# Performance work log

Measured on AMD Instinct MI355X. Metric: run time of the kernel, lower is better.

The kernel has to match this reference:

```python
import jax, jax.numpy as jnp
import numpy as np
import math

B, T, C, H = 2, 2048, 1024, 16

def setup_inputs() -> dict:
    key = jax.random.key(0)
    ks = jax.random.split(key, 5)
    s = 0.02
    return {
        "x": jax.random.normal(ks[0], (B, T, C), dtype=jnp.float32),
        "W_attn": jax.random.normal(ks[1], (C, 3 * C), dtype=jnp.float32) * s,
        "b_attn": jnp.zeros((3 * C,), dtype=jnp.float32),
        "W_proj": jax.random.normal(ks[2], (C, C), dtype=jnp.float32) * s,
        "b_proj": jnp.zeros((C,), dtype=jnp.float32),
    }

def reference(x, W_attn, b_attn, W_proj, b_proj):
    Bx, Tx, Cx = x.shape
    hd = Cx // H  # head dim = 64
    qkv = x @ W_attn + b_attn                      # [B,T,3C]
    q, k, v = jnp.split(qkv, 3, axis=-1)
    # [B,H,T,hd]
    q = q.reshape(Bx, Tx, H, hd).transpose(0, 2, 1, 3)
    k = k.reshape(Bx, Tx, H, hd).transpose(0, 2, 1, 3)
    v = v.reshape(Bx, Tx, H, hd).transpose(0, 2, 1, 3)
    scale = 1.0 / math.sqrt(hd)
    att = jnp.einsum('bhqd,bhkd->bhqk', q, k) * scale   # [B,H,T,T]
    causal = jnp.tril(jnp.ones((Tx, Tx), dtype=bool))
    att = jnp.where(causal[None, None, :, :], att, -jnp.inf)
    att = jax.nn.softmax(att, axis=-1)
    y = jnp.einsum('bhqk,bhkd->bhqd', att, v)           # [B,H,T,hd]
    y = y.transpose(0, 2, 1, 3).reshape(Bx, Tx, Cx)
    return y @ W_proj + b_proj
```

## Files before the change

### kernel.cpp

```cpp
#include <hip/hip_runtime.h>

typedef __attribute__((ext_vector_type(8))) __bf16 bf16x8;
typedef __attribute__((ext_vector_type(4))) float f32x4;

#define T_SEQ 2048
#define NH 16
#define HD 64
#define CDIM 1024
#define NQK 2048
#define NQKV 3072
#define MTOT 4096

#define SWZ(r, c) ((((r) * 8) + ((c) ^ ((r) & 7))) * 8)

__device__ __forceinline__ void async_load16(const void* g, void* l) {
    __builtin_amdgcn_global_load_lds(
        (const __attribute__((address_space(1))) void*)g,
        (__attribute__((address_space(3))) void*)l, 16, 0, 0);
}

__global__ __launch_bounds__(256) void cvt_bf16_kernel(const float* __restrict__ in,
                                                       __bf16* __restrict__ out, int n) {
    int i = (blockIdx.x * 256 + threadIdx.x) * 8;
    if (i + 8 <= n) {
        float4 f0 = *(const float4*)(in + i);
        float4 f1 = *(const float4*)(in + i + 4);
        bf16x8 o;
        o[0] = (__bf16)f0.x; o[1] = (__bf16)f0.y; o[2] = (__bf16)f0.z; o[3] = (__bf16)f0.w;
        o[4] = (__bf16)f1.x; o[5] = (__bf16)f1.y; o[6] = (__bf16)f1.z; o[7] = (__bf16)f1.w;
        *(bf16x8*)(out + i) = o;
    }
}

__global__ __launch_bounds__(256) void transpose2_kernel(
    const float* __restrict__ Wa, const float* __restrict__ Wp,
    __bf16* __restrict__ WaT, __bf16* __restrict__ WpT) {
    __shared__ float tile[32][33];
    const float* in; __bf16* out; int C, bx = blockIdx.x;
    if (bx < 96) { in = Wa; out = WaT; C = 3072; }
    else         { in = Wp; out = WpT; C = 1024; bx -= 96; }
    int c0 = bx * 32, r0 = blockIdx.y * 32;
    int tx = threadIdx.x, ty = threadIdx.y;
#pragma unroll
    for (int i = 0; i < 4; i++)
        tile[ty + i * 8][tx] = in[(size_t)(r0 + ty + i * 8) * C + c0 + tx];
    __syncthreads();
#pragma unroll
    for (int i = 0; i < 4; i++)
        out[(size_t)(c0 + ty + i * 8) * 1024 + r0 + tx] = (__bf16)tile[tx][ty + i * 8];
}

template <int WNW>
__global__ __launch_bounds__(256) void gemm_bt_kernel(
    const __bf16* __restrict__ A, const __bf16* __restrict__ Bt,
    const float* __restrict__ bias, int M, int N, int K, int mode,
    __bf16* __restrict__ qkb, __bf16* __restrict__ vtb, float* __restrict__ outf)
{
    constexpr int MI = (WNW == 2) ? 4 : 2;
    constexpr int BROWS = WNW * 64;
    __shared__ __bf16 As[128 * 64];
    __shared__ __bf16 Bs[BROWS * 64];

    int tid = threadIdx.x;
    int lane = tid & 63, wid = tid >> 6;
    int quad = lane >> 4, r16 = lane & 15;
    int wm = (WNW == 2) ? (wid >> 1) * 64 : wid * 32;
    int wn = (WNW == 2) ? (wid & 1) * 64 : 0;
    int bm = blockIdx.y * 128, bn = blockIdx.x * (WNW * 64);

    f32x4 acc[MI][4] = {};

    int lrow = lane >> 3;
    int lcolsw = (((lane & 7) ^ (lrow & 7)) * 8);
    const __bf16* Ag = A + (size_t)(bm + wid * 32 + lrow) * K + lcolsw;
    const __bf16* Bg = Bt + (size_t)(bn + wid * (BROWS / 4) + lrow) * K + lcolsw;
    char* lA = (char*)As + wid * 4096;
    char* lB = (char*)Bs + wid * (BROWS / 4) * 128;

    for (int kt = 0; kt < K; kt += 64) {
        __syncthreads();
#pragma unroll
        for (int i = 0; i < 4; i++)
            async_load16(Ag + kt + (size_t)i * 8 * K, lA + i * 1024);
#pragma unroll
        for (int i = 0; i < BROWS / 32; i++)
            async_load16(Bg + kt + (size_t)i * 8 * K, lB + i * 1024);
        __syncthreads();
#pragma unroll
        for (int ks = 0; ks < 2; ks++) {
            bf16x8 af[MI], bfr[4];
#pragma unroll
            for (int i = 0; i < MI; i++)
                af[i] = *(const bf16x8*)&As[SWZ(wm + i * 16 + r16, ks * 4 + quad)];
#pragma unroll
            for (int i = 0; i < 4; i++)
                bfr[i] = *(const bf16x8*)&Bs[SWZ(wn + i * 16 + r16, ks * 4 + quad)];
#pragma unroll
            for (int mi = 0; mi < MI; mi++)
#pragma unroll
                for (int ni = 0; ni < 4; ni++)
                    acc[mi][ni] = __builtin_amdgcn_mfma_f32_16x16x32_bf16(
                        af[mi], bfr[ni], acc[mi][ni], 0, 0, 0);
        }
    }

    const float SC2 = 0.125f * 1.44269504088896f;
#pragma unroll
    for (int mi = 0; mi < MI; mi++) {
#pragma unroll
        for (int ni = 0; ni < 4; ni++) {
            int col = bn + wn + ni * 16 + r16;
            float bv = bias[col];
            int row0 = bm + wm + mi * 16 + quad * 4;
            if (mode == 1) {
#pragma unroll
                for (int rg = 0; rg < 4; rg++)
                    outf[(size_t)(row0 + rg) * N + col] = acc[mi][ni][rg] + bv;
            } else if (col < 1024) {
#pragma unroll
                for (int rg = 0; rg < 4; rg++)
                    qkb[(size_t)(row0 + rg) * NQK + col] = (__bf16)((acc[mi][ni][rg] + bv) * SC2);
            } else if (col < 2048) {
#pragma unroll
                for (int rg = 0; rg < 4; rg++)
                    qkb[(size_t)(row0 + rg) * NQK + col] = (__bf16)(acc[mi][ni][rg] + bv);
            } else {
                int dcol = col - 2048;
                int b = row0 >> 11, t0 = row0 & 2047;
                union { __bf16 h[4]; uint2 u; } pk;
#pragma unroll
                for (int rg = 0; rg < 4; rg++) pk.h[rg] = (__bf16)(acc[mi][ni][rg] + bv);
                *(uint2*)&vtb[((size_t)b * 1024 + dcol) * T_SEQ + t0] = pk.u;
            }
        }
    }
}

__global__ __launch_bounds__(256) void attn_kernel(
    const __bf16* __restrict__ qkb, const __bf16* __restrict__ vtb,
    __bf16* __restrict__ y1)
{
    __shared__ __bf16 Ks[2][64 * 64];
    __shared__ __bf16 Vs[2][64 * 64];
    __shared__ __bf16 Ps[2][4][16][72];

    int tid = threadIdx.x;
    int lane = tid & 63, w = tid >> 6;
    int quad = lane >> 4, r16 = lane & 15;
    int bh = blockIdx.y;
    int b = bh >> 4, h = bh & 15;
    int qtA = blockIdx.x, qtB = 31 - qtA;
    int qbA = qtA * 64, qbB = qtB * 64;

    const __bf16* Qh = qkb + (size_t)b * T_SEQ * NQK + h * HD;
    const __bf16* Kh = Qh + CDIM;
    const __bf16* Vh = vtb + ((size_t)b * 1024 + h * HD) * T_SEQ;

    const float NEG_INF = -__builtin_inff();
    int lrow = lane >> 3;
    int lcolsw = (((lane & 7) ^ (lrow & 7)) * 8);

    bf16x8 qfA[2], qfB[2];
#pragma unroll
    for (int ks = 0; ks < 2; ks++) {
        qfA[ks] = *(const bf16x8*)(Qh + (size_t)(qbA + w * 16 + r16) * NQK + ks * 32 + quad * 8);
        qfB[ks] = *(const bf16x8*)(Qh + (size_t)(qbB + w * 16 + r16) * NQK + ks * 32 + quad * 8);
    }

    bf16x8 onesv;
#pragma unroll
    for (int i = 0; i < 8; i++) onesv[i] = (__bf16)1.0f;

    f32x4 oA[4] = {}, oB[4] = {};
    f32x4 lA4 = {}, lB4 = {};
    int g0A = qbA + w * 16, g0B = qbB + w * 16;
    int qrowA = g0A + r16, qrowB = g0B + r16;

    auto stage = [&](int kt, int buf) {
        int kb = kt * 64;
        char* lK = (char*)Ks[buf] + w * 2048;
        char* lV = (char*)Vs[buf] + w * 2048;
        const __bf16* kg = Kh + (size_t)(kb + w * 16 + lrow) * NQK + lcolsw;
        const __bf16* vg = Vh + (size_t)(w * 16 + lrow) * T_SEQ + kb + lcolsw;
        async_load16(kg, lK);
        async_load16(kg + (size_t)8 * NQK, lK + 1024);
        async_load16(vg, lV);
        async_load16(vg + (size_t)8 * T_SEQ, lV + 1024);
    };

    auto softmax_store = [&](f32x4 (&s)[4], int qrow, int kb, bool diag, int slot) {
        if (diag) {
#pragma unroll
            for (int ni = 0; ni < 4; ni++)
#pragma unroll
                for (int rg = 0; rg < 4; rg++)
                    if (kb + ni * 16 + quad * 4 + rg > qrow) s[ni][rg] = NEG_INF;
        }
#pragma unroll
        for (int ni = 0; ni < 4; ni++) {
            union { __bf16 h[4]; uint2 u; } pk;
#pragma unroll
            for (int rg = 0; rg < 4; rg++)
                pk.h[rg] = (__bf16)__builtin_amdgcn_exp2f(s[ni][rg]);
            *(uint2*)&Ps[slot][w][r16][ni * 16 + quad * 4] = pk.u;
        }
    };

    int nktA = qtA + 1, nktB = qtB + 1;
    stage(0, 0);
    int cur = 0;
    for (int kt = 0; kt < nktB; kt++) {
        __syncthreads();
        if (kt + 1 < nktB) stage(kt + 1, cur ^ 1);
        const bool doA = (kt < nktA);
        const int kb = kt * 64;

        f32x4 sB[4] = {}, sA[4] = {};
#pragma unroll
        for (int ks = 0; ks < 2; ks++) {
            bf16x8 kf[4];
#pragma unroll
            for (int ni = 0; ni < 4; ni++)
                kf[ni] = *(const bf16x8*)&Ks[cur][SWZ(ni * 16 + r16, ks * 4 + quad)];
            __builtin_amdgcn_s_setprio(1);
#pragma unroll
            for (int ni = 0; ni < 4; ni++)
                sB[ni] = __builtin_amdgcn_mfma_f32_16x16x32_bf16(kf[ni], qfB[ks], sB[ni], 0, 0, 0);
            if (doA) {
#pragma unroll
                for (int ni = 0; ni < 4; ni++)
                    sA[ni] = __builtin_amdgcn_mfma_f32_16x16x32_bf16(kf[ni], qfA[ks], sA[ni], 0, 0, 0);
            }
            __builtin_amdgcn_s_setprio(0);
        }

        softmax_store(sB, qrowB, kb, kb + 63 > g0B, 1);
        if (doA) softmax_store(sA, qrowA, kb, kb + 63 > g0A, 0);

#pragma unroll
        for (int ks = 0; ks < 2; ks++) {
            bf16x8 vf[4];
#pragma unroll
            for (int nd = 0; nd < 4; nd++)
                vf[nd] = *(const bf16x8*)&Vs[cur][SWZ(nd * 16 + r16, ks * 4 + quad)];
            bf16x8 pbB = *(const bf16x8*)&Ps[1][w][r16][ks * 32 + quad * 8];
            __builtin_amdgcn_s_setprio(1);
#pragma unroll
            for (int nd = 0; nd < 4; nd++)
                oB[nd] = __builtin_amdgcn_mfma_f32_16x16x32_bf16(vf[nd], pbB, oB[nd], 0, 0, 0);
            lB4 = __builtin_amdgcn_mfma_f32_16x16x32_bf16(onesv, pbB, lB4, 0, 0, 0);
            __builtin_amdgcn_s_setprio(0);
            if (doA) {
                bf16x8 pbA = *(const bf16x8*)&Ps[0][w][r16][ks * 32 + quad * 8];
                __builtin_amdgcn_s_setprio(1);
#pragma unroll
                for (int nd = 0; nd < 4; nd++)
                    oA[nd] = __builtin_amdgcn_mfma_f32_16x16x32_bf16(vf[nd], pbA, oA[nd], 0, 0, 0);
                lA4 = __builtin_amdgcn_mfma_f32_16x16x32_bf16(onesv, pbA, lA4, 0, 0, 0);
                __builtin_amdgcn_s_setprio(0);
            }
        }
        cur ^= 1;
    }

#pragma unroll
    for (int which = 0; which < 2; which++) {
        f32x4* o = which ? oB : oA;
        float inv = 1.f / (which ? lB4[0] : lA4[0]);
        int t = (which ? qbB : qbA) + w * 16 + r16;
#pragma unroll
        for (int nd = 0; nd < 4; nd++) {
            union { __bf16 h[4]; uint2 u; } pk;
#pragma unroll
            for (int rg = 0; rg < 4; rg++) pk.h[rg] = (__bf16)(o[nd][rg] * inv);
            *(uint2*)&y1[(size_t)(b * T_SEQ + t) * CDIM + h * HD + nd * 16 + quad * 4] = pk.u;
        }
    }
}

extern "C" void kernel_launch(void* const* d_in, const int* in_sizes, int n_in,
                              void* d_out, int out_size, void* d_ws, size_t ws_size,
                              hipStream_t stream) {
    const float* x = (const float*)d_in[0];
    const float* W_attn = (const float*)d_in[1];
    const float* b_attn = (const float*)d_in[2];
    const float* W_proj = (const float*)d_in[3];
    const float* b_proj = (const float*)d_in[4];
    float* out = (float*)d_out;

    char* p = (char*)d_ws;
    __bf16* xb = (__bf16*)p;   p += (size_t)MTOT * CDIM * 2;
    __bf16* WaT = (__bf16*)p;  p += (size_t)3 * CDIM * CDIM * 2;
    __bf16* WpT = (__bf16*)p;  p += (size_t)CDIM * CDIM * 2;
    __bf16* qkb = (__bf16*)p;  p += (size_t)MTOT * NQK * 2;
    __bf16* vtb = (__bf16*)p;  p += (size_t)2 * 1024 * T_SEQ * 2;
    __bf16* y1 = xb;

    cvt_bf16_kernel<<<2048, 256, 0, stream>>>(x, xb, MTOT * CDIM);
    transpose2_kernel<<<dim3(128, 32), dim3(32, 8), 0, stream>>>(W_attn, W_proj, WaT, WpT);
    gemm_bt_kernel<2><<<dim3(24, 32), 256, 0, stream>>>(xb, WaT, b_attn, MTOT, NQKV, CDIM, 0,
                                                        qkb, vtb, nullptr);
    attn_kernel<<<dim3(16, 32), 256, 0, stream>>>(qkb, vtb, y1);
    gemm_bt_kernel<1><<<dim3(16, 32), 256, 0, stream>>>(y1, WpT, b_proj, MTOT, CDIM, CDIM, 1,
                                                        nullptr, nullptr, out);
}
```

Baseline: 185.7 us.

## Split attention key range across two blocks with a combine kernel

Splits each query-tile pair's key loop across two blocks using strided tiles, which doubles the attention grid from 512 to 1024 blocks to fill more compute units. Each block writes unnormalized fp32 partial outputs and row sums to workspace, and a new combine kernel adds the two partials, normalizes, and writes bf16. Softmax uses no running max, so the partials can simply be summed. The cost is extra workspace traffic (about 33 MB of fp32 partials written and then read) plus one more kernel launch, and the split only activates when the workspace is large enough.

```diff
diff --git a/kernel.cpp b/kernel.cpp
--- a/kernel.cpp
+++ b/kernel.cpp
@@ -138,7 +138,8 @@
 
 __global__ __launch_bounds__(256) void attn_kernel(
     const __bf16* __restrict__ qkb, const __bf16* __restrict__ vtb,
-    __bf16* __restrict__ y1)
+    __bf16* __restrict__ y1, float* __restrict__ opart, float* __restrict__ lpart,
+    int nsplit)
 {
     __shared__ __bf16 Ks[2][64 * 64];
     __shared__ __bf16 Vs[2][64 * 64];
@@ -149,7 +150,9 @@
     int quad = lane >> 4, r16 = lane & 15;
     int bh = blockIdx.y;
     int b = bh >> 4, h = bh & 15;
-    int qtA = blockIdx.x, qtB = 31 - qtA;
+    int pairIdx = blockIdx.x / nsplit;
+    int half = blockIdx.x - pairIdx * nsplit;
+    int qtA = pairIdx, qtB = 31 - pairIdx;
     int qbA = qtA * 64, qbB = qtB * 64;
 
     const __bf16* Qh = qkb + (size_t)b * T_SEQ * NQK + h * HD;
@@ -207,11 +210,11 @@
     };
 
     int nktA = qtA + 1, nktB = qtB + 1;
-    stage(0, 0);
+    stage(half, 0);
     int cur = 0;
-    for (int kt = 0; kt < nktB; kt++) {
+    for (int kt = half; kt < nktB; kt += nsplit) {
         __syncthreads();
-        if (kt + 1 < nktB) stage(kt + 1, cur ^ 1);
+        if (kt + nsplit < nktB) stage(kt + nsplit, cur ^ 1);
         const bool doA = (kt < nktA);
         const int kb = kt * 64;
 
@@ -263,19 +266,59 @@
         cur ^= 1;
     }
 
-#pragma unroll
-    for (int which = 0; which < 2; which++) {
-        f32x4* o = which ? oB : oA;
-        float inv = 1.f / (which ? lB4[0] : lA4[0]);
-        int t = (which ? qbB : qbA) + w * 16 + r16;
-#pragma unroll
-        for (int nd = 0; nd < 4; nd++) {
-            union { __bf16 h[4]; uint2 u; } pk;
-#pragma unroll
-            for (int rg = 0; rg < 4; rg++) pk.h[rg] = (__bf16)(o[nd][rg] * inv);
-            *(uint2*)&y1[(size_t)(b * T_SEQ + t) * CDIM + h * HD + nd * 16 + quad * 4] = pk.u;
-        }
-    }
+    if (nsplit == 1) {
+#pragma unroll
+        for (int which = 0; which < 2; which++) {
+            f32x4* o = which ? oB : oA;
+            float inv = 1.f / (which ? lB4[0] : lA4[0]);
+            int t = (which ? qbB : qbA) + w * 16 + r16;
+#pragma unroll
+            for (int nd = 0; nd < 4; nd++) {
+                union { __bf16 h4[4]; uint2 u; } pk;
+#pragma unroll
+                for (int rg = 0; rg < 4; rg++) pk.h4[rg] = (__bf16)(o[nd][rg] * inv);
+                *(uint2*)&y1[(size_t)(b * T_SEQ + t) * CDIM + h * HD + nd * 16 + quad * 4] = pk.u;
+            }
+        }
+    } else {
+#pragma unroll
+        for (int which = 0; which < 2; which++) {
+            f32x4* o = which ? oB : oA;
+            int qb = which ? qbB : qbA;
+            int t = qb + w * 16 + r16;
+            size_t rbase = (((size_t)half * 32 + bh) * T_SEQ + t) * 64 + quad * 4;
+#pragma unroll
+            for (int nd = 0; nd < 4; nd++)
+                *(f32x4*)&opart[rbase + nd * 16] = o[nd];
+            if (lane < 16)
+                lpart[((size_t)half * 32 + bh) * T_SEQ + qb + w * 16 + lane] =
+                    which ? lB4[0] : lA4[0];
+        }
+    }
+}
+
+__global__ __launch_bounds__(256) void attn_combine_kernel(
+    const float* __restrict__ opart, const float* __restrict__ lpart,
+    __bf16* __restrict__ y1)
+{
+    const size_t HSTR = (size_t)32 * T_SEQ * 64;
+    const size_t LSTR = (size_t)32 * T_SEQ;
+    int i4 = blockIdx.x * 256 + threadIdx.x;
+    int dc = (i4 & 15) * 4;
+    int t = (i4 >> 4) & (T_SEQ - 1);
+    int bh = i4 >> 15;
+    size_t base = ((size_t)bh * T_SEQ + t) * 64 + dc;
+    f32x4 a = *(const f32x4*)&opart[base];
+    f32x4 c = *(const f32x4*)&opart[HSTR + base];
+    float l = lpart[(size_t)bh * T_SEQ + t] + lpart[LSTR + (size_t)bh * T_SEQ + t];
+    float inv = 1.f / l;
+    int b = bh >> 4, h = bh & 15;
+    union { __bf16 h4[4]; uint2 u; } pk;
+    pk.h4[0] = (__bf16)((a[0] + c[0]) * inv);
+    pk.h4[1] = (__bf16)((a[1] + c[1]) * inv);
+    pk.h4[2] = (__bf16)((a[2] + c[2]) * inv);
+    pk.h4[3] = (__bf16)((a[3] + c[3]) * inv);
+    *(uint2*)&y1[((size_t)(b * T_SEQ + t)) * CDIM + h * HD + dc] = pk.u;
 }
 
 extern "C" void kernel_launch(void* const* d_in, const int* in_sizes, int n_in,
@@ -294,13 +337,20 @@
     __bf16* WpT = (__bf16*)p;  p += (size_t)CDIM * CDIM * 2;
     __bf16* qkb = (__bf16*)p;  p += (size_t)MTOT * NQK * 2;
     __bf16* vtb = (__bf16*)p;  p += (size_t)2 * 1024 * T_SEQ * 2;
+    float* opart = (float*)p;  p += (size_t)2 * 32 * T_SEQ * 64 * 4;
+    float* lpart = (float*)p;  p += (size_t)2 * 32 * T_SEQ * 4;
     __bf16* y1 = xb;
+
+    size_t ws_needed = (size_t)(p - (char*)d_ws);
+    int nsplit = (ws_size >= ws_needed) ? 2 : 1;
 
     cvt_bf16_kernel<<<2048, 256, 0, stream>>>(x, xb, MTOT * CDIM);
     transpose2_kernel<<<dim3(128, 32), dim3(32, 8), 0, stream>>>(W_attn, W_proj, WaT, WpT);
     gemm_bt_kernel<2><<<dim3(24, 32), 256, 0, stream>>>(xb, WaT, b_attn, MTOT, NQKV, CDIM, 0,
                                                         qkb, vtb, nullptr);
-    attn_kernel<<<dim3(16, 32), 256, 0, stream>>>(qkb, vtb, y1);
+    attn_kernel<<<dim3(16 * nsplit, 32), 256, 0, stream>>>(qkb, vtb, y1, opart, lpart, nsplit);
+    if (nsplit == 2)
+        attn_combine_kernel<<<4096, 256, 0, stream>>>(opart, lpart, y1);
     gemm_bt_kernel<1><<<dim3(16, 32), 256, 0, stream>>>(y1, WpT, b_proj, MTOT, CDIM, CDIM, 1,
                                                         nullptr, nullptr, out);
 }
```

New measurement: 191.2 us. 1.03x slower.
